# Kernel optimization log

Hardware: AMD Instinct MI355X
Metric: run time of the kernel (lower is better)

The kernel has to match this reference:

```python
import jax, jax.numpy as jnp
import numpy as np


def setup_inputs() -> dict:
    key = jax.random.key(0)
    k1, k2, k3, k4, k5 = jax.random.split(key, 5)
    B, H, W, C, F = 8, 64, 64, 256, 64
    # glorot_uniform for 1x1 conv kernels [1,1,Cin,Cout]
    def glorot(k, cin, cout):
        lim = float(np.sqrt(6.0 / (cin + cout)))
        return jax.random.uniform(k, (1, 1, cin, cout), jnp.float32, -lim, lim)
    x = jax.random.normal(k1, (B, H, W, C), dtype=jnp.float32)
    Wf = glorot(k2, C, F)
    Wg = glorot(k3, C, F)
    Wh = glorot(k4, C, C)
    Wv = glorot(k5, C, C)
    gamma = jnp.zeros((1,), dtype=jnp.float32) + 0.1  # nonzero so attention path matters
    return {"x": x, "Wf": Wf, "Wg": Wg, "Wh": Wh, "Wv": Wv, "gamma": gamma}


def reference(x, Wf, Wg, Wh, Wv, gamma):
    B, H, W, C = x.shape
    N = H * W
    # 1x1 convs are pointwise matmuls over channels
    f = jnp.einsum('bhwc,cf->bhwf', x, Wf[0, 0])   # [B,H,W,F]
    g = jnp.einsum('bhwc,cf->bhwf', x, Wg[0, 0])   # [B,H,W,F]
    h = jnp.einsum('bhwc,cd->bhwd', x, Wh[0, 0])   # [B,H,W,C]
    ff = f.reshape(B, N, -1)                        # [B,N,F]
    gf = g.reshape(B, N, -1)                        # [B,N,F]
    hf = h.reshape(B, N, C)                         # [B,N,C]
    # s[b,i,j] = ff[b,i,:] . gf[b,j,:]  (no 1/sqrt(d) scaling, as in source)
    s = jnp.einsum('bif,bjf->bij', ff, gf)          # [B,N,N]
    beta = jax.nn.softmax(s, axis=-1)
    o = jnp.einsum('bij,bjc->bic', beta, hf)        # [B,N,C]
    o = o.reshape(B, H, W, C)
    o = jnp.einsum('bhwc,cd->bhwd', o, Wv[0, 0])
    return gamma * o + x
```

## Files before the change

### kernel.cpp

```cpp
#include <hip/hip_runtime.h>

typedef _Float16 half8   __attribute__((ext_vector_type(8)));
typedef _Float16 half4_t __attribute__((ext_vector_type(4)));
typedef float    float4_t __attribute__((ext_vector_type(4)));

#define B_   8
#define N_   4096
#define C_   256
#define F_   64

static __device__ __forceinline__ float4_t mfma16(half8 a, half8 b, float4_t c) {
  return __builtin_amdgcn_mfma_f32_16x16x32_f16(a, b, c, 0, 0, 0);
}

__global__ __launch_bounds__(256) void prep_whvt(const float* __restrict__ Wh,
                                                 const float* __restrict__ Wv,
                                                 _Float16* __restrict__ whvt) {
  int d = blockIdx.x;
  int c = threadIdx.x;
  const float4_t* whr = (const float4_t*)(Wh + (size_t)c * 256);
  float acc = 0.f;
#pragma unroll 8
  for (int e4 = 0; e4 < 64; ++e4) {
    float4_t w4 = whr[e4];
    acc += w4[0] * Wv[(e4 * 4 + 0) * 256 + d];
    acc += w4[1] * Wv[(e4 * 4 + 1) * 256 + d];
    acc += w4[2] * Wv[(e4 * 4 + 2) * 256 + d];
    acc += w4[3] * Wv[(e4 * 4 + 3) * 256 + d];
  }
  whvt[d * 256 + c] = (_Float16)acc;
}

__global__ __launch_bounds__(256) void prep_wfgt(const float* __restrict__ Wf,
                                                 const float* __restrict__ Wg,
                                                 _Float16* __restrict__ wfgt) {
  int n = blockIdx.x;
  int c = threadIdx.x;
  float v = (n < 64) ? Wf[c * 64 + n] : Wg[c * 64 + (n - 64)];
  wfgt[n * 256 + c] = (_Float16)v;
}

__global__ __launch_bounds__(256) void transpose_x(const float* __restrict__ x,
                                                   _Float16* __restrict__ xT) {
  __shared__ float tile[32][33];
  int b  = blockIdx.x >> 7;
  int n0 = (blockIdx.x & 127) << 5;
  int c0 = blockIdx.y << 5;
  int tid = threadIdx.x;
  int r  = tid >> 3;
  int cc = (tid & 7) << 2;
  const float* src = x + ((size_t)(b * N_ + n0 + r)) * C_ + c0 + cc;
  float4_t v = *(const float4_t*)src;
  tile[r][cc + 0] = v[0]; tile[r][cc + 1] = v[1];
  tile[r][cc + 2] = v[2]; tile[r][cc + 3] = v[3];
  __syncthreads();
  half4_t o;
  o[0] = (_Float16)tile[cc + 0][r];
  o[1] = (_Float16)tile[cc + 1][r];
  o[2] = (_Float16)tile[cc + 2][r];
  o[3] = (_Float16)tile[cc + 3][r];
  _Float16* dst = xT + ((size_t)(b * C_ + c0 + r)) * N_ + n0 + cc;
  *(half4_t*)dst = o;
}

__global__ __launch_bounds__(256) void fg_kernel(const float* __restrict__ x,
                                                 const _Float16* __restrict__ wfgt,
                                                 _Float16* __restrict__ f,
                                                 _Float16* __restrict__ g) {
  int tid  = threadIdx.x;
  int wave = tid >> 6, lane = tid & 63;
  int n16  = lane & 15, quad = lane >> 4;
  int row  = blockIdx.x * 64 + wave * 16 + n16;
  float4_t acc[8];
#pragma unroll
  for (int t = 0; t < 8; t++) acc[t] = (float4_t){0.f, 0.f, 0.f, 0.f};
  for (int k0 = 0; k0 < 256; k0 += 32) {
    const float* xp = x + (size_t)row * C_ + k0 + quad * 8;
    float4_t x0 = *(const float4_t*)xp;
    float4_t x1 = *(const float4_t*)(xp + 4);
    half8 af;
#pragma unroll
    for (int j = 0; j < 4; j++) { af[j] = (_Float16)x0[j]; af[4 + j] = (_Float16)x1[j]; }
#pragma unroll
    for (int t = 0; t < 8; t++) {
      half8 bf = *(const half8*)(wfgt + (size_t)(t * 16 + n16) * 256 + k0 + quad * 8);
      acc[t] = mfma16(af, bf, acc[t]);
    }
  }
  int orow = blockIdx.x * 64 + wave * 16 + quad * 4;
#pragma unroll
  for (int t = 0; t < 8; t++) {
#pragma unroll
    for (int r = 0; r < 4; r++) {
      _Float16 v = (_Float16)acc[t][r];
      int col = t * 16 + n16;
      if (t < 4) f[(size_t)(orow + r) * 64 + col] = v;
      else       g[(size_t)(orow + r) * 64 + col - 64] = v;
    }
  }
}

__global__ __launch_bounds__(256, 2) void flash_kernel(const _Float16* __restrict__ f,
                                                       const _Float16* __restrict__ g,
                                                       const _Float16* __restrict__ xT,
                                                       _Float16* __restrict__ a) {
  __shared__ _Float16 ktb2[2][64 * 64];
  __shared__ _Float16 ptb2[2][64 * 64];
  __shared__ float alpha_lds[2][64];
  __shared__ float linv_lds[64];

  const int b   = blockIdx.x;
  const int i0  = blockIdx.y * 64;
  const int tid = threadIdx.x;
  const int wave = tid >> 6, lane = tid & 63;
  const int n16 = lane & 15, quad = lane >> 4;
  const int nlo = n16 & 7, nhi = n16 >> 3;

  half8 qf[2];
  {
    const _Float16* qp = f + (size_t)(b * N_ + i0 + wave * 16 + n16) * 64 + quad * 8;
    qf[0] = *(const half8*)qp;
    qf[1] = *(const half8*)(qp + 32);
  }

  float4_t o_acc[16];
#pragma unroll
  for (int t = 0; t < 16; t++) o_acc[t] = (float4_t){0.f, 0.f, 0.f, 0.f};
  float m_i[4] = {-1e30f, -1e30f, -1e30f, -1e30f};
  float l_i[4] = {0.f, 0.f, 0.f, 0.f};

  const _Float16* gbase = g + (size_t)(b * N_) * 64;
  const _Float16* xbase = xT + ((size_t)b * C_ + 64 * wave) * (size_t)N_;

  const int krow = tid >> 2;
  const int kcb  = (tid & 3) << 1;
  const int krb  = krow & 7;

  {
    const _Float16* ks = gbase + (size_t)krow * 64 + (kcb << 3);
    half8 k0 = *(const half8*)ks;
    half8 k1 = *(const half8*)(ks + 8);
    _Float16* kd = ktb2[0] + krow * 64;
    *(half8*)(kd + (((kcb    ) ^ krb) << 3)) = k0;
    *(half8*)(kd + (((kcb + 1) ^ krb) << 3)) = k1;
  }
  __syncthreads();

  for (int k = 0; k < 64; ++k) {
    const int j0  = k << 6;
    const int buf = k & 1;
    const int j0n = (j0 + 64) & (N_ - 1);

    half8 kp0, kp1;
    {
      const _Float16* ks = gbase + (size_t)(j0n + krow) * 64 + (kcb << 3);
      kp0 = *(const half8*)ks;
      kp1 = *(const half8*)(ks + 8);
    }
    half8 vfr[8];
#pragma unroll
    for (int s = 0; s < 2; s++)
#pragma unroll
      for (int ct = 0; ct < 4; ct++)
        vfr[s * 4 + ct] = *(const half8*)(xbase + (size_t)(16 * ct + n16) * N_ +
                                          j0 + 32 * s + 8 * quad);

    float4_t s_acc[4];
#pragma unroll
    for (int t = 0; t < 4; t++) s_acc[t] = (float4_t){0.f, 0.f, 0.f, 0.f};
    {
      const _Float16* ktb = ktb2[buf];
#pragma unroll
      for (int s = 0; s < 2; s++)
#pragma unroll
        for (int t = 0; t < 4; t++) {
          half8 bf = *(const half8*)(ktb + (16 * t + n16) * 64 +
                                     (((4 * s + quad) ^ nlo) << 3));
          s_acc[t] = mfma16(qf[s], bf, s_acc[t]);
        }
    }

    float alpha_r[4];
#pragma unroll
    for (int r = 0; r < 4; r++) {
      float v = fmaxf(fmaxf(s_acc[0][r], s_acc[1][r]),
                      fmaxf(s_acc[2][r], s_acc[3][r]));
#pragma unroll
      for (int d = 1; d < 16; d <<= 1)
        v = fmaxf(v, __shfl_xor(v, d, 16));
      float mn = fmaxf(m_i[r], v);
      alpha_r[r] = __expf(m_i[r] - mn);
      m_i[r] = mn;
    }
    _Float16* pb = ptb2[buf];
#pragma unroll
    for (int r = 0; r < 4; r++) {
      float s0 = __expf(s_acc[0][r] - m_i[r]);
      float s1 = __expf(s_acc[1][r] - m_i[r]);
      float s2 = __expf(s_acc[2][r] - m_i[r]);
      float s3 = __expf(s_acc[3][r] - m_i[r]);
      float v = s0 + s1 + s2 + s3;
#pragma unroll
      for (int d = 1; d < 16; d <<= 1)
        v += __shfl_xor(v, d, 16);
      l_i[r] = l_i[r] * alpha_r[r] + v;
      const int row = wave * 16 + 4 * quad + r;
      const int rb  = row & 7;
      _Float16* pr = pb + row * 64 + nlo;
      pr[((nhi    ) ^ rb) << 3] = (_Float16)s0;
      pr[((nhi + 2) ^ rb) << 3] = (_Float16)s1;
      pr[((nhi + 4) ^ rb) << 3] = (_Float16)s2;
      pr[((nhi + 6) ^ rb) << 3] = (_Float16)s3;
    }
    if (n16 == 0) {
#pragma unroll
      for (int r = 0; r < 4; r++)
        alpha_lds[buf][wave * 16 + 4 * quad + r] = alpha_r[r];
    }
    {
      _Float16* kd = ktb2[buf ^ 1] + krow * 64;
      *(half8*)(kd + (((kcb    ) ^ krb) << 3)) = kp0;
      *(half8*)(kd + (((kcb + 1) ^ krb) << 3)) = kp1;
    }
    __syncthreads();

#pragma unroll
    for (int ti = 0; ti < 4; ti++)
#pragma unroll
      for (int r = 0; r < 4; r++) {
        float al = alpha_lds[buf][ti * 16 + 4 * quad + r];
#pragma unroll
        for (int ct = 0; ct < 4; ct++) o_acc[ti * 4 + ct][r] *= al;
      }

#pragma unroll
    for (int s = 0; s < 2; s++)
#pragma unroll
      for (int ti = 0; ti < 4; ti++) {
        half8 af = *(const half8*)(pb + (16 * ti + n16) * 64 +
                                   (((4 * s + quad) ^ nlo) << 3));
#pragma unroll
        for (int ct = 0; ct < 4; ct++)
          o_acc[ti * 4 + ct] = mfma16(af, vfr[s * 4 + ct], o_acc[ti * 4 + ct]);
      }
  }

  if (n16 == 0) {
#pragma unroll
    for (int r = 0; r < 4; r++)
      linv_lds[wave * 16 + 4 * quad + r] = 1.f / l_i[r];
  }
  __syncthreads();
#pragma unroll
  for (int ti = 0; ti < 4; ti++)
#pragma unroll
    for (int r = 0; r < 4; r++) {
      float il = linv_lds[ti * 16 + 4 * quad + r];
      size_t orow = (size_t)(b * N_ + i0 + ti * 16 + 4 * quad + r) * C_;
#pragma unroll
      for (int ct = 0; ct < 4; ct++)
        a[orow + 64 * wave + 16 * ct + n16] =
            (_Float16)(o_acc[ti * 4 + ct][r] * il);
    }
}

__global__ __launch_bounds__(256) void out_kernel(const _Float16* __restrict__ a,
                                                  const _Float16* __restrict__ whvt,
                                                  const float* __restrict__ x,
                                                  const float* __restrict__ gamma,
                                                  float* __restrict__ out) {
  int tid  = threadIdx.x;
  int wave = tid >> 6, lane = tid & 63;
  int n16  = lane & 15, quad = lane >> 4;
  int row  = blockIdx.x * 64 + wave * 16 + n16;
  float4_t acc[16];
#pragma unroll
  for (int t = 0; t < 16; t++) acc[t] = (float4_t){0.f, 0.f, 0.f, 0.f};
  for (int k0 = 0; k0 < 256; k0 += 32) {
    half8 af = *(const half8*)(a + (size_t)row * C_ + k0 + quad * 8);
#pragma unroll
    for (int t = 0; t < 16; t++) {
      half8 bf = *(const half8*)(whvt + (size_t)(t * 16 + n16) * 256 + k0 + quad * 8);
      acc[t] = mfma16(af, bf, acc[t]);
    }
  }
  float gm = gamma[0];
  int orow = blockIdx.x * 64 + wave * 16 + quad * 4;
#pragma unroll
  for (int t = 0; t < 16; t++) {
#pragma unroll
    for (int r = 0; r < 4; r++) {
      size_t idx = (size_t)(orow + r) * C_ + t * 16 + n16;
      out[idx] = gm * acc[t][r] + x[idx];
    }
  }
}

extern "C" void kernel_launch(void* const* d_in, const int* in_sizes, int n_in,
                              void* d_out, int out_size, void* d_ws, size_t ws_size,
                              hipStream_t stream) {
  const float* x     = (const float*)d_in[0];
  const float* Wf    = (const float*)d_in[1];
  const float* Wg    = (const float*)d_in[2];
  const float* Wh    = (const float*)d_in[3];
  const float* Wv    = (const float*)d_in[4];
  const float* gamma = (const float*)d_in[5];
  float* out = (float*)d_out;

  char* w = (char*)d_ws;
  _Float16* whvt = (_Float16*)(w);
  _Float16* wfgt = (_Float16*)(w + 131072);
  _Float16* fb   = (_Float16*)(w + 196608);
  _Float16* gb   = (_Float16*)(w + 196608 + 4194304);
  _Float16* xT   = (_Float16*)(w + 196608 + 2 * 4194304);
  _Float16* ab   = (_Float16*)(w + 196608 + 2 * 4194304 + 16777216);

  hipLaunchKernelGGL(prep_whvt,  dim3(256),     dim3(256), 0, stream, Wh, Wv, whvt);
  hipLaunchKernelGGL(prep_wfgt,  dim3(128),     dim3(256), 0, stream, Wf, Wg, wfgt);
  hipLaunchKernelGGL(transpose_x,dim3(1024, 8), dim3(256), 0, stream, x, xT);
  hipLaunchKernelGGL(fg_kernel,  dim3(512),     dim3(256), 0, stream, x, wfgt, fb, gb);
  hipLaunchKernelGGL(flash_kernel, dim3(8, 64), dim3(256), 0, stream, fb, gb, xT, ab);
  hipLaunchKernelGGL(out_kernel, dim3(512),     dim3(256), 0, stream, ab, whvt, x, gamma, out);
}
```

Measured before the change: 293.2 us.

## Split flash attention KV range across two wave groups and merge partial softmax

The flash kernel now runs 512 threads per block, and each half handles half of the key/value sequence with its own double-buffered LDS tiles. The two partial results are merged at the end using their max and sum statistics, passed through shared memory. It also skips the rescale of the output accumulator when every alpha in the tile equals one. Separately, the two weight-prep kernels are fused into one launch and out_kernel is split across two column halves for more blocks. This targets latency and under-occupancy in the sequential KV loop, at the cost of more LDS, an extra reduction pass, and higher register pressure under launch_bounds(512,4).

Result: slower. 723.6 us (+146.8%).

```diff
diff --git a/kernel.cpp b/kernel.cpp
--- a/kernel.cpp
+++ b/kernel.cpp
@@ -13,31 +13,32 @@
   return __builtin_amdgcn_mfma_f32_16x16x32_f16(a, b, c, 0, 0, 0);
 }
 
-__global__ __launch_bounds__(256) void prep_whvt(const float* __restrict__ Wh,
-                                                 const float* __restrict__ Wv,
-                                                 _Float16* __restrict__ whvt) {
-  int d = blockIdx.x;
+__global__ __launch_bounds__(256) void prep_weights(const float* __restrict__ Wh,
+                                                    const float* __restrict__ Wv,
+                                                    const float* __restrict__ Wf,
+                                                    const float* __restrict__ Wg,
+                                                    _Float16* __restrict__ whvt,
+                                                    _Float16* __restrict__ wfgt) {
+  int blk = blockIdx.x;
   int c = threadIdx.x;
-  const float4_t* whr = (const float4_t*)(Wh + (size_t)c * 256);
-  float acc = 0.f;
+  if (blk < 256) {
+    int d = blk;
+    const float4_t* whr = (const float4_t*)(Wh + (size_t)c * 256);
+    float acc = 0.f;
 #pragma unroll 8
-  for (int e4 = 0; e4 < 64; ++e4) {
-    float4_t w4 = whr[e4];
-    acc += w4[0] * Wv[(e4 * 4 + 0) * 256 + d];
-    acc += w4[1] * Wv[(e4 * 4 + 1) * 256 + d];
-    acc += w4[2] * Wv[(e4 * 4 + 2) * 256 + d];
-    acc += w4[3] * Wv[(e4 * 4 + 3) * 256 + d];
-  }
-  whvt[d * 256 + c] = (_Float16)acc;
-}
-
-__global__ __launch_bounds__(256) void prep_wfgt(const float* __restrict__ Wf,
-                                                 const float* __restrict__ Wg,
-                                                 _Float16* __restrict__ wfgt) {
-  int n = blockIdx.x;
-  int c = threadIdx.x;
-  float v = (n < 64) ? Wf[c * 64 + n] : Wg[c * 64 + (n - 64)];
-  wfgt[n * 256 + c] = (_Float16)v;
+    for (int e4 = 0; e4 < 64; ++e4) {
+      float4_t w4 = whr[e4];
+      acc += w4[0] * Wv[(e4 * 4 + 0) * 256 + d];
+      acc += w4[1] * Wv[(e4 * 4 + 1) * 256 + d];
+      acc += w4[2] * Wv[(e4 * 4 + 2) * 256 + d];
+      acc += w4[3] * Wv[(e4 * 4 + 3) * 256 + d];
+    }
+    whvt[d * 256 + c] = (_Float16)acc;
+  } else {
+    int n = blk - 256;
+    float v = (n < 64) ? Wf[c * 64 + n] : Wg[c * 64 + (n - 64)];
+    wfgt[n * 256 + c] = (_Float16)v;
+  }
 }
 
 __global__ __launch_bounds__(256) void transpose_x(const float* __restrict__ x,
@@ -100,25 +101,30 @@
   }
 }
 
-__global__ __launch_bounds__(256, 2) void flash_kernel(const _Float16* __restrict__ f,
+__global__ __launch_bounds__(512, 4) void flash_kernel(const _Float16* __restrict__ f,
                                                        const _Float16* __restrict__ g,
                                                        const _Float16* __restrict__ xT,
                                                        _Float16* __restrict__ a) {
-  __shared__ _Float16 ktb2[2][64 * 64];
-  __shared__ _Float16 ptb2[2][64 * 64];
-  __shared__ float alpha_lds[2][64];
-  __shared__ float linv_lds[64];
+  __shared__ _Float16 smem[32768];
+  __shared__ float alpha_lds[2][2][64];
+  __shared__ float m_lds[2][64], l_lds[2][64];
+  __shared__ int   skipf[2][2][4];
 
   const int b   = blockIdx.x;
   const int i0  = blockIdx.y * 64;
   const int tid = threadIdx.x;
-  const int wave = tid >> 6, lane = tid & 63;
+  const int wave = tid >> 6;
+  const int half = wave >> 2, wh = wave & 3;
+  const int lane = tid & 63;
   const int n16 = lane & 15, quad = lane >> 4;
   const int nlo = n16 & 7, nhi = n16 >> 3;
 
+  _Float16* kt0 = smem + half * 2 * 4096;
+  _Float16* pt0 = smem + 16384 + half * 2 * 4096;
+
   half8 qf[2];
   {
-    const _Float16* qp = f + (size_t)(b * N_ + i0 + wave * 16 + n16) * 64 + quad * 8;
+    const _Float16* qp = f + (size_t)(b * N_ + i0 + wh * 16 + n16) * 64 + quad * 8;
     qf[0] = *(const half8*)qp;
     qf[1] = *(const half8*)(qp + 32);
   }
@@ -129,31 +135,33 @@
   float m_i[4] = {-1e30f, -1e30f, -1e30f, -1e30f};
   float l_i[4] = {0.f, 0.f, 0.f, 0.f};
 
-  const _Float16* gbase = g + (size_t)(b * N_) * 64;
-  const _Float16* xbase = xT + ((size_t)b * C_ + 64 * wave) * (size_t)N_;
-
-  const int krow = tid >> 2;
-  const int kcb  = (tid & 3) << 1;
+  const int jbase = half * 2048;
+  const _Float16* gbase = g + (size_t)(b * N_ + jbase) * 64;
+  const _Float16* xbase = xT + ((size_t)b * C_ + 64 * wh) * (size_t)N_;
+
+  const int htid = tid & 255;
+  const int krow = htid >> 2;
+  const int kcb  = (htid & 3) << 1;
   const int krb  = krow & 7;
 
   {
     const _Float16* ks = gbase + (size_t)krow * 64 + (kcb << 3);
-    half8 k0 = *(const half8*)ks;
-    half8 k1 = *(const half8*)(ks + 8);
-    _Float16* kd = ktb2[0] + krow * 64;
-    *(half8*)(kd + (((kcb    ) ^ krb) << 3)) = k0;
-    *(half8*)(kd + (((kcb + 1) ^ krb) << 3)) = k1;
+    half8 k0v = *(const half8*)ks;
+    half8 k1v = *(const half8*)(ks + 8);
+    _Float16* kd = kt0 + krow * 64;
+    *(half8*)(kd + (((kcb    ) ^ krb) << 3)) = k0v;
+    *(half8*)(kd + (((kcb + 1) ^ krb) << 3)) = k1v;
   }
   __syncthreads();
 
-  for (int k = 0; k < 64; ++k) {
-    const int j0  = k << 6;
+  for (int k = 0; k < 32; ++k) {
     const int buf = k & 1;
-    const int j0n = (j0 + 64) & (N_ - 1);
+    const int j0  = jbase + (k << 6);
+    const int kn  = (k + 1) & 31;
 
     half8 kp0, kp1;
     {
-      const _Float16* ks = gbase + (size_t)(j0n + krow) * 64 + (kcb << 3);
+      const _Float16* ks = gbase + (size_t)((kn << 6) + krow) * 64 + (kcb << 3);
       kp0 = *(const half8*)ks;
       kp1 = *(const half8*)(ks + 8);
     }
@@ -169,7 +177,7 @@
 #pragma unroll
     for (int t = 0; t < 4; t++) s_acc[t] = (float4_t){0.f, 0.f, 0.f, 0.f};
     {
-      const _Float16* ktb = ktb2[buf];
+      const _Float16* ktb = kt0 + buf * 4096;
 #pragma unroll
       for (int s = 0; s < 2; s++)
 #pragma unroll
@@ -192,7 +200,7 @@
       alpha_r[r] = __expf(m_i[r] - mn);
       m_i[r] = mn;
     }
-    _Float16* pb = ptb2[buf];
+    _Float16* pb = pt0 + buf * 4096;
 #pragma unroll
     for (int r = 0; r < 4; r++) {
       float s0 = __expf(s_acc[0][r] - m_i[r]);
@@ -204,7 +212,7 @@
       for (int d = 1; d < 16; d <<= 1)
         v += __shfl_xor(v, d, 16);
       l_i[r] = l_i[r] * alpha_r[r] + v;
-      const int row = wave * 16 + 4 * quad + r;
+      const int row = wh * 16 + 4 * quad + r;
       const int rb  = row & 7;
       _Float16* pr = pb + row * 64 + nlo;
       pr[((nhi    ) ^ rb) << 3] = (_Float16)s0;
@@ -215,23 +223,32 @@
     if (n16 == 0) {
 #pragma unroll
       for (int r = 0; r < 4; r++)
-        alpha_lds[buf][wave * 16 + 4 * quad + r] = alpha_r[r];
-    }
+        alpha_lds[half][buf][wh * 16 + 4 * quad + r] = alpha_r[r];
+    }
+    int aok = (alpha_r[0] == 1.f) && (alpha_r[1] == 1.f) &&
+              (alpha_r[2] == 1.f) && (alpha_r[3] == 1.f);
+    int wall = __all(aok);
+    if (lane == 0) skipf[half][buf][wh] = wall;
+
     {
-      _Float16* kd = ktb2[buf ^ 1] + krow * 64;
+      _Float16* kd = kt0 + (buf ^ 1) * 4096 + krow * 64;
       *(half8*)(kd + (((kcb    ) ^ krb) << 3)) = kp0;
       *(half8*)(kd + (((kcb + 1) ^ krb) << 3)) = kp1;
     }
     __syncthreads();
 
-#pragma unroll
-    for (int ti = 0; ti < 4; ti++)
-#pragma unroll
-      for (int r = 0; r < 4; r++) {
-        float al = alpha_lds[buf][ti * 16 + 4 * quad + r];
-#pragma unroll
-        for (int ct = 0; ct < 4; ct++) o_acc[ti * 4 + ct][r] *= al;
-      }
+    int sk = skipf[half][buf][0] & skipf[half][buf][1] &
+             skipf[half][buf][2] & skipf[half][buf][3];
+    if (!sk) {
+#pragma unroll
+      for (int ti = 0; ti < 4; ti++)
+#pragma unroll
+        for (int r = 0; r < 4; r++) {
+          float al = alpha_lds[half][buf][ti * 16 + 4 * quad + r];
+#pragma unroll
+          for (int ct = 0; ct < 4; ct++) o_acc[ti * 4 + ct][r] *= al;
+        }
+    }
 
 #pragma unroll
     for (int s = 0; s < 2; s++)
@@ -247,21 +264,56 @@
 
   if (n16 == 0) {
 #pragma unroll
-    for (int r = 0; r < 4; r++)
-      linv_lds[wave * 16 + 4 * quad + r] = 1.f / l_i[r];
+    for (int r = 0; r < 4; r++) {
+      m_lds[half][wh * 16 + 4 * quad + r] = m_i[r];
+      l_lds[half][wh * 16 + 4 * quad + r] = l_i[r];
+    }
   }
   __syncthreads();
+
+  float cw[16];
 #pragma unroll
   for (int ti = 0; ti < 4; ti++)
 #pragma unroll
     for (int r = 0; r < 4; r++) {
-      float il = linv_lds[ti * 16 + 4 * quad + r];
-      size_t orow = (size_t)(b * N_ + i0 + ti * 16 + 4 * quad + r) * C_;
-#pragma unroll
-      for (int ct = 0; ct < 4; ct++)
-        a[orow + 64 * wave + 16 * ct + n16] =
-            (_Float16)(o_acc[ti * 4 + ct][r] * il);
-    }
+      int row = ti * 16 + 4 * quad + r;
+      float m1 = m_lds[0][row], l1 = l_lds[0][row];
+      float m2 = m_lds[1][row], l2 = l_lds[1][row];
+      float mm = fmaxf(m1, m2);
+      float u1 = __expf(m1 - mm), u2 = __expf(m2 - mm);
+      float dn = u1 * l1 + u2 * l2;
+      cw[ti * 4 + r] = (half ? u2 : u1) / dn;
+    }
+
+  _Float16* cmb = smem;
+  if (half == 1) {
+#pragma unroll
+    for (int ti = 0; ti < 4; ti++)
+#pragma unroll
+      for (int r = 0; r < 4; r++) {
+        int row = ti * 16 + 4 * quad + r;
+#pragma unroll
+        for (int ct = 0; ct < 4; ct++)
+          cmb[row * 256 + 64 * wh + 16 * ct + n16] =
+              (_Float16)(o_acc[ti * 4 + ct][r] * cw[ti * 4 + r]);
+      }
+  }
+  __syncthreads();
+  if (half == 0) {
+#pragma unroll
+    for (int ti = 0; ti < 4; ti++)
+#pragma unroll
+      for (int r = 0; r < 4; r++) {
+        int row = ti * 16 + 4 * quad + r;
+        size_t orow = (size_t)(b * N_ + i0 + row) * C_;
+#pragma unroll
+        for (int ct = 0; ct < 4; ct++) {
+          float v = o_acc[ti * 4 + ct][r] * cw[ti * 4 + r] +
+                    (float)cmb[row * 256 + 64 * wh + 16 * ct + n16];
+          a[orow + 64 * wh + 16 * ct + n16] = (_Float16)v;
+        }
+      }
+  }
 }
 
 __global__ __launch_bounds__(256) void out_kernel(const _Float16* __restrict__ a,
@@ -272,25 +324,27 @@
   int tid  = threadIdx.x;
   int wave = tid >> 6, lane = tid & 63;
   int n16  = lane & 15, quad = lane >> 4;
+  int colh = blockIdx.y;
   int row  = blockIdx.x * 64 + wave * 16 + n16;
-  float4_t acc[16];
-#pragma unroll
-  for (int t = 0; t < 16; t++) acc[t] = (float4_t){0.f, 0.f, 0.f, 0.f};
+  float4_t acc[8];
+#pragma unroll
+  for (int t = 0; t < 8; t++) acc[t] = (float4_t){0.f, 0.f, 0.f, 0.f};
   for (int k0 = 0; k0 < 256; k0 += 32) {
     half8 af = *(const half8*)(a + (size_t)row * C_ + k0 + quad * 8);
 #pragma unroll
-    for (int t = 0; t < 16; t++) {
-      half8 bf = *(const half8*)(whvt + (size_t)(t * 16 + n16) * 256 + k0 + quad * 8);
+    for (int t = 0; t < 8; t++) {
+      half8 bf = *(const half8*)(whvt + (size_t)(colh * 128 + t * 16 + n16) * 256 +
+                                 k0 + quad * 8);
       acc[t] = mfma16(af, bf, acc[t]);
     }
   }
   float gm = gamma[0];
   int orow = blockIdx.x * 64 + wave * 16 + quad * 4;
 #pragma unroll
-  for (int t = 0; t < 16; t++) {
-#pragma unroll
-    for (int r = 0; r < 4; r++) {
-      size_t idx = (size_t)(orow + r) * C_ + t * 16 + n16;
+  for (int t = 0; t < 8; t++) {
+#pragma unroll
+    for (int r = 0; r < 4; r++) {
+      size_t idx = (size_t)(orow + r) * C_ + colh * 128 + t * 16 + n16;
       out[idx] = gm * acc[t][r] + x[idx];
     }
   }
@@ -315,10 +369,10 @@
   _Float16* xT   = (_Float16*)(w + 196608 + 2 * 4194304);
   _Float16* ab   = (_Float16*)(w + 196608 + 2 * 4194304 + 16777216);
 
-  hipLaunchKernelGGL(prep_whvt,  dim3(256),     dim3(256), 0, stream, Wh, Wv, whvt);
-  hipLaunchKernelGGL(prep_wfgt,  dim3(128),     dim3(256), 0, stream, Wf, Wg, wfgt);
-  hipLaunchKernelGGL(transpose_x,dim3(1024, 8), dim3(256), 0, stream, x, xT);
-  hipLaunchKernelGGL(fg_kernel,  dim3(512),     dim3(256), 0, stream, x, wfgt, fb, gb);
-  hipLaunchKernelGGL(flash_kernel, dim3(8, 64), dim3(256), 0, stream, fb, gb, xT, ab);
-  hipLaunchKernelGGL(out_kernel, dim3(512),     dim3(256), 0, stream, ab, whvt, x, gamma, out);
-}
+  hipLaunchKernelGGL(prep_weights, dim3(384),    dim3(256), 0, stream,
+                     Wh, Wv, Wf, Wg, whvt, wfgt);
+  hipLaunchKernelGGL(transpose_x,  dim3(1024, 8),dim3(256), 0, stream, x, xT);
+  hipLaunchKernelGGL(fg_kernel,    dim3(512),    dim3(256), 0, stream, x, wfgt, fb, gb);
+  hipLaunchKernelGGL(flash_kernel, dim3(8, 64),  dim3(512), 0, stream, fb, gb, xT, ab);
+  hipLaunchKernelGGL(out_kernel,   dim3(512, 2), dim3(256), 0, stream, ab, whvt, x, gamma, out);
+}
```

## Split flash attention over key halves, merge in output GEMM, fuse prep kernels

Applied to the files above, without the earlier changes.

Merges the three prep kernels into a single launch and splits the flash attention across two key-range halves via gridDim.z. Each half writes partial normalized outputs plus row max and sum, and the output kernel merges them with softmax-style rescaling before the Wh·Wv projection. The output kernel is also split across two column halves. Inside flash, the row sum is computed with an MFMA against a ones vector instead of shuffles, the rescale is skipped when no row max changed, and occupancy is raised to 4 blocks. The extra cost is more workspace traffic for the two partial buffers, fp16 rounding in the merge, and a dependence on workspace size to turn the split on.

New measurement: 911.8 us. +211.0%, slower.

```diff
diff --git a/kernel.cpp b/kernel.cpp
--- a/kernel.cpp
+++ b/kernel.cpp
@@ -13,54 +13,55 @@
   return __builtin_amdgcn_mfma_f32_16x16x32_f16(a, b, c, 0, 0, 0);
 }
 
-__global__ __launch_bounds__(256) void prep_whvt(const float* __restrict__ Wh,
-                                                 const float* __restrict__ Wv,
-                                                 _Float16* __restrict__ whvt) {
-  int d = blockIdx.x;
-  int c = threadIdx.x;
-  const float4_t* whr = (const float4_t*)(Wh + (size_t)c * 256);
-  float acc = 0.f;
+__global__ __launch_bounds__(256) void prep_all(const float* __restrict__ x,
+                                                const float* __restrict__ Wh,
+                                                const float* __restrict__ Wv,
+                                                const float* __restrict__ Wf,
+                                                const float* __restrict__ Wg,
+                                                _Float16* __restrict__ xT,
+                                                _Float16* __restrict__ whvt,
+                                                _Float16* __restrict__ wfgt) {
+  __shared__ float tile[32][33];
+  int blk = blockIdx.x;
+  int tid = threadIdx.x;
+  if (blk < 8192) {
+    int b  = (blk & 1023) >> 7;
+    int n0 = (blk & 127) << 5;
+    int c0 = (blk >> 10) << 5;
+    int r  = tid >> 3;
+    int cc = (tid & 7) << 2;
+    const float* src = x + ((size_t)(b * N_ + n0 + r)) * C_ + c0 + cc;
+    float4_t v = *(const float4_t*)src;
+    tile[r][cc + 0] = v[0]; tile[r][cc + 1] = v[1];
+    tile[r][cc + 2] = v[2]; tile[r][cc + 3] = v[3];
+    __syncthreads();
+    half4_t o;
+    o[0] = (_Float16)tile[cc + 0][r];
+    o[1] = (_Float16)tile[cc + 1][r];
+    o[2] = (_Float16)tile[cc + 2][r];
+    o[3] = (_Float16)tile[cc + 3][r];
+    _Float16* dst = xT + ((size_t)(b * C_ + c0 + r)) * N_ + n0 + cc;
+    *(half4_t*)dst = o;
+  } else if (blk < 8448) {
+    int d = blk - 8192;
+    int c = tid;
+    const float4_t* whr = (const float4_t*)(Wh + (size_t)c * 256);
+    float acc = 0.f;
 #pragma unroll 8
-  for (int e4 = 0; e4 < 64; ++e4) {
-    float4_t w4 = whr[e4];
-    acc += w4[0] * Wv[(e4 * 4 + 0) * 256 + d];
-    acc += w4[1] * Wv[(e4 * 4 + 1) * 256 + d];
-    acc += w4[2] * Wv[(e4 * 4 + 2) * 256 + d];
-    acc += w4[3] * Wv[(e4 * 4 + 3) * 256 + d];
-  }
-  whvt[d * 256 + c] = (_Float16)acc;
-}
-
-__global__ __launch_bounds__(256) void prep_wfgt(const float* __restrict__ Wf,
-                                                 const float* __restrict__ Wg,
-                                                 _Float16* __restrict__ wfgt) {
-  int n = blockIdx.x;
-  int c = threadIdx.x;
-  float v = (n < 64) ? Wf[c * 64 + n] : Wg[c * 64 + (n - 64)];
-  wfgt[n * 256 + c] = (_Float16)v;
-}
-
-__global__ __launch_bounds__(256) void transpose_x(const float* __restrict__ x,
-                                                   _Float16* __restrict__ xT) {
-  __shared__ float tile[32][33];
-  int b  = blockIdx.x >> 7;
-  int n0 = (blockIdx.x & 127) << 5;
-  int c0 = blockIdx.y << 5;
-  int tid = threadIdx.x;
-  int r  = tid >> 3;
-  int cc = (tid & 7) << 2;
-  const float* src = x + ((size_t)(b * N_ + n0 + r)) * C_ + c0 + cc;
-  float4_t v = *(const float4_t*)src;
-  tile[r][cc + 0] = v[0]; tile[r][cc + 1] = v[1];
-  tile[r][cc + 2] = v[2]; tile[r][cc + 3] = v[3];
-  __syncthreads();
-  half4_t o;
-  o[0] = (_Float16)tile[cc + 0][r];
-  o[1] = (_Float16)tile[cc + 1][r];
-  o[2] = (_Float16)tile[cc + 2][r];
-  o[3] = (_Float16)tile[cc + 3][r];
-  _Float16* dst = xT + ((size_t)(b * C_ + c0 + r)) * N_ + n0 + cc;
-  *(half4_t*)dst = o;
+    for (int e4 = 0; e4 < 64; ++e4) {
+      float4_t w4 = whr[e4];
+      acc += w4[0] * Wv[(e4 * 4 + 0) * 256 + d];
+      acc += w4[1] * Wv[(e4 * 4 + 1) * 256 + d];
+      acc += w4[2] * Wv[(e4 * 4 + 2) * 256 + d];
+      acc += w4[3] * Wv[(e4 * 4 + 3) * 256 + d];
+    }
+    whvt[d * 256 + c] = (_Float16)acc;
+  } else {
+    int n = blk - 8448;
+    int c = tid;
+    float v = (n < 64) ? Wf[c * 64 + n] : Wg[c * 64 + (n - 64)];
+    wfgt[n * 256 + c] = (_Float16)v;
+  }
 }
 
 __global__ __launch_bounds__(256) void fg_kernel(const float* __restrict__ x,
@@ -100,17 +101,23 @@
   }
 }
 
-__global__ __launch_bounds__(256, 2) void flash_kernel(const _Float16* __restrict__ f,
+__global__ __launch_bounds__(256, 4) void flash_kernel(const _Float16* __restrict__ f,
                                                        const _Float16* __restrict__ g,
                                                        const _Float16* __restrict__ xT,
-                                                       _Float16* __restrict__ a) {
+                                                       _Float16* __restrict__ a1,
+                                                       _Float16* __restrict__ a2,
+                                                       float2* __restrict__ mlb) {
   __shared__ _Float16 ktb2[2][64 * 64];
   __shared__ _Float16 ptb2[2][64 * 64];
   __shared__ float alpha_lds[2][64];
-  __shared__ float linv_lds[64];
+  __shared__ float l_lds[64];
+  __shared__ int   skipf[2][4];
 
   const int b   = blockIdx.x;
   const int i0  = blockIdx.y * 64;
+  const int jh  = blockIdx.z;
+  const int iters = (N_ / 64) / gridDim.z;
+  const int jbase = jh * (N_ / gridDim.z);
   const int tid = threadIdx.x;
   const int wave = tid >> 6, lane = tid & 63;
   const int n16 = lane & 15, quad = lane >> 4;
@@ -122,14 +129,20 @@
     qf[0] = *(const half8*)qp;
     qf[1] = *(const half8*)(qp + 32);
   }
+  half8 onesb;
+  {
+    _Float16 ov = (n16 == 0) ? (_Float16)1.f : (_Float16)0.f;
+#pragma unroll
+    for (int j = 0; j < 8; j++) onesb[j] = ov;
+  }
 
   float4_t o_acc[16];
 #pragma unroll
   for (int t = 0; t < 16; t++) o_acc[t] = (float4_t){0.f, 0.f, 0.f, 0.f};
+  float4_t lacc = (float4_t){0.f, 0.f, 0.f, 0.f};
   float m_i[4] = {-1e30f, -1e30f, -1e30f, -1e30f};
-  float l_i[4] = {0.f, 0.f, 0.f, 0.f};
-
-  const _Float16* gbase = g + (size_t)(b * N_) * 64;
+
+  const _Float16* gbase = g + (size_t)(b * N_ + jbase) * 64;
   const _Float16* xbase = xT + ((size_t)b * C_ + 64 * wave) * (size_t)N_;
 
   const int krow = tid >> 2;
@@ -138,22 +151,22 @@
 
   {
     const _Float16* ks = gbase + (size_t)krow * 64 + (kcb << 3);
-    half8 k0 = *(const half8*)ks;
-    half8 k1 = *(const half8*)(ks + 8);
+    half8 k0v = *(const half8*)ks;
+    half8 k1v = *(const half8*)(ks + 8);
     _Float16* kd = ktb2[0] + krow * 64;
-    *(half8*)(kd + (((kcb    ) ^ krb) << 3)) = k0;
-    *(half8*)(kd + (((kcb + 1) ^ krb) << 3)) = k1;
+    *(half8*)(kd + (((kcb    ) ^ krb) << 3)) = k0v;
+    *(half8*)(kd + (((kcb + 1) ^ krb) << 3)) = k1v;
   }
   __syncthreads();
 
-  for (int k = 0; k < 64; ++k) {
-    const int j0  = k << 6;
+  for (int k = 0; k < iters; ++k) {
     const int buf = k & 1;
-    const int j0n = (j0 + 64) & (N_ - 1);
+    const int j0  = jbase + (k << 6);
+    const int kn  = (k + 1) & (iters - 1);
 
     half8 kp0, kp1;
     {
-      const _Float16* ks = gbase + (size_t)(j0n + krow) * 64 + (kcb << 3);
+      const _Float16* ks = gbase + (size_t)((kn << 6) + krow) * 64 + (kcb << 3);
       kp0 = *(const half8*)ks;
       kp1 = *(const half8*)(ks + 8);
     }
@@ -199,11 +212,6 @@
       float s1 = __expf(s_acc[1][r] - m_i[r]);
       float s2 = __expf(s_acc[2][r] - m_i[r]);
       float s3 = __expf(s_acc[3][r] - m_i[r]);
-      float v = s0 + s1 + s2 + s3;
-#pragma unroll
-      for (int d = 1; d < 16; d <<= 1)
-        v += __shfl_xor(v, d, 16);
-      l_i[r] = l_i[r] * alpha_r[r] + v;
       const int row = wave * 16 + 4 * quad + r;
       const int rb  = row & 7;
       _Float16* pr = pb + row * 64 + nlo;
@@ -217,6 +225,11 @@
       for (int r = 0; r < 4; r++)
         alpha_lds[buf][wave * 16 + 4 * quad + r] = alpha_r[r];
     }
+    int aok = (alpha_r[0] == 1.f) && (alpha_r[1] == 1.f) &&
+              (alpha_r[2] == 1.f) && (alpha_r[3] == 1.f);
+    int wall = __all(aok);
+    if (lane == 0) skipf[buf][wave] = wall;
+
     {
       _Float16* kd = ktb2[buf ^ 1] + krow * 64;
       *(half8*)(kd + (((kcb    ) ^ krb) << 3)) = kp0;
@@ -224,14 +237,20 @@
     }
     __syncthreads();
 
-#pragma unroll
-    for (int ti = 0; ti < 4; ti++)
-#pragma unroll
-      for (int r = 0; r < 4; r++) {
-        float al = alpha_lds[buf][ti * 16 + 4 * quad + r];
-#pragma unroll
-        for (int ct = 0; ct < 4; ct++) o_acc[ti * 4 + ct][r] *= al;
+    int sk = skipf[buf][0] & skipf[buf][1] & skipf[buf][2] & skipf[buf][3];
+    if (!sk) {
+#pragma unroll
+      for (int ti = 0; ti < 4; ti++) {
+#pragma unroll
+        for (int r = 0; r < 4; r++) {
+          float al = alpha_lds[buf][ti * 16 + 4 * quad + r];
+#pragma unroll
+          for (int ct = 0; ct < 4; ct++) o_acc[ti * 4 + ct][r] *= al;
+        }
       }
+#pragma unroll
+      for (int r = 0; r < 4; r++) lacc[r] *= alpha_r[r];
+    }
 
 #pragma unroll
     for (int s = 0; s < 2; s++)
@@ -239,6 +258,7 @@
       for (int ti = 0; ti < 4; ti++) {
         half8 af = *(const half8*)(pb + (16 * ti + n16) * 64 +
                                    (((4 * s + quad) ^ nlo) << 3));
+        if (ti == wave) lacc = mfma16(af, onesb, lacc);
 #pragma unroll
         for (int ct = 0; ct < 4; ct++)
           o_acc[ti * 4 + ct] = mfma16(af, vfr[s * 4 + ct], o_acc[ti * 4 + ct]);
@@ -247,50 +267,82 @@
 
   if (n16 == 0) {
 #pragma unroll
-    for (int r = 0; r < 4; r++)
-      linv_lds[wave * 16 + 4 * quad + r] = 1.f / l_i[r];
+    for (int r = 0; r < 4; r++) {
+      int row = wave * 16 + 4 * quad + r;
+      l_lds[row] = lacc[r];
+      mlb[((size_t)(b * 2 + jh)) * N_ + i0 + row] = make_float2(m_i[r], lacc[r]);
+    }
   }
   __syncthreads();
+
+  _Float16* ap = jh ? a2 : a1;
 #pragma unroll
   for (int ti = 0; ti < 4; ti++)
 #pragma unroll
     for (int r = 0; r < 4; r++) {
-      float il = linv_lds[ti * 16 + 4 * quad + r];
-      size_t orow = (size_t)(b * N_ + i0 + ti * 16 + 4 * quad + r) * C_;
+      int row = ti * 16 + 4 * quad + r;
+      float il = 1.f / l_lds[row];
+      size_t orow = (size_t)(b * N_ + i0 + row) * C_;
 #pragma unroll
       for (int ct = 0; ct < 4; ct++)
-        a[orow + 64 * wave + 16 * ct + n16] =
+        ap[orow + 64 * wave + 16 * ct + n16] =
             (_Float16)(o_acc[ti * 4 + ct][r] * il);
     }
 }
 
-__global__ __launch_bounds__(256) void out_kernel(const _Float16* __restrict__ a,
+__global__ __launch_bounds__(256) void out_kernel(const _Float16* __restrict__ a1,
+                                                  const _Float16* __restrict__ a2,
+                                                  const float2* __restrict__ mlb,
                                                   const _Float16* __restrict__ whvt,
                                                   const float* __restrict__ x,
                                                   const float* __restrict__ gamma,
-                                                  float* __restrict__ out) {
+                                                  float* __restrict__ out,
+                                                  int jsplit) {
   int tid  = threadIdx.x;
   int wave = tid >> 6, lane = tid & 63;
   int n16  = lane & 15, quad = lane >> 4;
+  int colh = blockIdx.y;
   int row  = blockIdx.x * 64 + wave * 16 + n16;
-  float4_t acc[16];
-#pragma unroll
-  for (int t = 0; t < 16; t++) acc[t] = (float4_t){0.f, 0.f, 0.f, 0.f};
+
+  _Float16 c1h = (_Float16)1.f, c2h = (_Float16)0.f;
+  if (jsplit == 2) {
+    int b = row >> 12, i = row & (N_ - 1);
+    float2 ml1 = mlb[((size_t)(b * 2 + 0)) * N_ + i];
+    float2 ml2 = mlb[((size_t)(b * 2 + 1)) * N_ + i];
+    float mm = fmaxf(ml1.x, ml2.x);
+    float u1 = __expf(ml1.x - mm) * ml1.y;
+    float u2 = __expf(ml2.x - mm) * ml2.y;
+    float dn = u1 + u2;
+    c1h = (_Float16)(u1 / dn);
+    c2h = (_Float16)(u2 / dn);
+  }
+
+  float4_t acc[8];
+#pragma unroll
+  for (int t = 0; t < 8; t++) acc[t] = (float4_t){0.f, 0.f, 0.f, 0.f};
   for (int k0 = 0; k0 < 256; k0 += 32) {
-    half8 af = *(const half8*)(a + (size_t)row * C_ + k0 + quad * 8);
-#pragma unroll
-    for (int t = 0; t < 16; t++) {
-      half8 bf = *(const half8*)(whvt + (size_t)(t * 16 + n16) * 256 + k0 + quad * 8);
+    half8 af;
+    if (jsplit == 2) {
+      half8 v1 = *(const half8*)(a1 + (size_t)row * C_ + k0 + quad * 8);
+      half8 v2 = *(const half8*)(a2 + (size_t)row * C_ + k0 + quad * 8);
+      af = v1 * c1h + v2 * c2h;
+    } else {
+      af = *(const half8*)(a1 + (size_t)row * C_ + k0 + quad * 8);
+    }
+#pragma unroll
+    for (int t = 0; t < 8; t++) {
+      half8 bf = *(const half8*)(whvt + (size_t)(colh * 128 + t * 16 + n16) * 256 +
+                                 k0 + quad * 8);
       acc[t] = mfma16(af, bf, acc[t]);
     }
   }
   float gm = gamma[0];
   int orow = blockIdx.x * 64 + wave * 16 + quad * 4;
 #pragma unroll
-  for (int t = 0; t < 16; t++) {
-#pragma unroll
-    for (int r = 0; r < 4; r++) {
-      size_t idx = (size_t)(orow + r) * C_ + t * 16 + n16;
+  for (int t = 0; t < 8; t++) {
+#pragma unroll
+    for (int r = 0; r < 4; r++) {
+      size_t idx = (size_t)(orow + r) * C_ + colh * 128 + t * 16 + n16;
       out[idx] = gm * acc[t][r] + x[idx];
     }
   }
@@ -308,17 +360,23 @@
   float* out = (float*)d_out;
 
   char* w = (char*)d_ws;
+  const size_t MB = 1024 * 1024;
   _Float16* whvt = (_Float16*)(w);
   _Float16* wfgt = (_Float16*)(w + 131072);
   _Float16* fb   = (_Float16*)(w + 196608);
-  _Float16* gb   = (_Float16*)(w + 196608 + 4194304);
-  _Float16* xT   = (_Float16*)(w + 196608 + 2 * 4194304);
-  _Float16* ab   = (_Float16*)(w + 196608 + 2 * 4194304 + 16777216);
-
-  hipLaunchKernelGGL(prep_whvt,  dim3(256),     dim3(256), 0, stream, Wh, Wv, whvt);
-  hipLaunchKernelGGL(prep_wfgt,  dim3(128),     dim3(256), 0, stream, Wf, Wg, wfgt);
-  hipLaunchKernelGGL(transpose_x,dim3(1024, 8), dim3(256), 0, stream, x, xT);
-  hipLaunchKernelGGL(fg_kernel,  dim3(512),     dim3(256), 0, stream, x, wfgt, fb, gb);
-  hipLaunchKernelGGL(flash_kernel, dim3(8, 64), dim3(256), 0, stream, fb, gb, xT, ab);
-  hipLaunchKernelGGL(out_kernel, dim3(512),     dim3(256), 0, stream, ab, whvt, x, gamma, out);
-}
+  _Float16* gb   = (_Float16*)(w + 196608 + 4 * MB);
+  _Float16* xT   = (_Float16*)(w + 196608 + 8 * MB);
+  _Float16* a1   = (_Float16*)(w + 196608 + 24 * MB);
+  _Float16* a2   = (_Float16*)(w + 196608 + 40 * MB);
+  float2*   mlb  = (float2*)  (w + 196608 + 56 * MB);
+
+  int jsplit = (ws_size >= (size_t)60 * MB) ? 2 : 1;
+
+  hipLaunchKernelGGL(prep_all, dim3(8576), dim3(256), 0, stream,
+                     x, Wh, Wv, Wf, Wg, xT, whvt, wfgt);
+  hipLaunchKernelGGL(fg_kernel, dim3(512), dim3(256), 0, stream, x, wfgt, fb, gb);
+  hipLaunchKernelGGL(flash_kernel, dim3(8, 64, jsplit), dim3(256), 0, stream,
+                     fb, gb, xT, a1, a2, mlb);
+  hipLaunchKernelGGL(out_kernel, dim3(512, 2), dim3(256), 0, stream,
+                     a1, a2, mlb, whvt, x, gamma, out, jsplit);
+}
```
